# Optimization experiments

Hardware: AMD Instinct MI355X
Metric: run time of the kernel (lower is better)

## Reference

```python
import jax, jax.numpy as jnp
import numpy as np

B, N, M = 16, 4096, 256
Q_DIM, CTX_DIM = 512, 768
HEADS, DIM_HEAD = 8, 64
INNER = HEADS * DIM_HEAD
SCALE = DIM_HEAD ** -0.5


def setup_inputs() -> dict:
    key = jax.random.key(0)
    ks = jax.random.split(key, 8)
    x = jax.random.normal(ks[0], (B, N, Q_DIM), dtype=jnp.float32)
    obj_txt = jax.random.normal(ks[1], (B, M, CTX_DIM), dtype=jnp.float32)
    obj_mask = jax.random.randint(ks[2], (B, N, M), 0, 2) > 0
    obj_vector = jnp.ones((B, M), dtype=bool)  # all-True keeps output finite (see notes)
    Wq = jax.random.normal(ks[3], (Q_DIM, INNER), dtype=jnp.float32) * 0.02
    Wk = jax.random.normal(ks[4], (CTX_DIM, INNER), dtype=jnp.float32) * 0.02
    Wv = jax.random.normal(ks[5], (CTX_DIM, INNER), dtype=jnp.float32) * 0.02
    Wo = jax.random.normal(ks[6], (INNER, Q_DIM), dtype=jnp.float32) * 0.02
    bo = jnp.zeros((Q_DIM,), dtype=jnp.float32)
    return {"x": x, "obj_txt": obj_txt, "obj_mask": obj_mask, "obj_vector": obj_vector,
            "Wq": Wq, "Wk": Wk, "Wv": Wv, "Wo": Wo, "bo": bo}


def reference(x, obj_txt, obj_mask, obj_vector, Wq, Wk, Wv, Wo, bo):
    b, n, _ = x.shape
    m = obj_txt.shape[1]
    q = (x @ Wq).reshape(b, n, HEADS, DIM_HEAD)          # [B,N,H,C]
    k = (obj_txt @ Wk).reshape(b, m, HEADS, DIM_HEAD)    # [B,M,H,C]
    v = (obj_txt @ Wv).reshape(b, m, HEADS, DIM_HEAD)
    sim = jnp.einsum('bnhc,bmhc->bhnm', q, k) * SCALE    # [B,H,N,M]
    neg = -jnp.finfo(sim.dtype).max
    # pre-softmax mask (obj_vector broadcasts over heads and queries)
    sim = jnp.where(obj_vector[:, None, None, :], sim, neg)
    # NOTE: original computes sim.softmax(-1) but then discards it, using the
    # pre-softmax masked sim with ~obj_mask positions set to 0 as the attention.
    attn = jnp.where(obj_mask[:, None, :, :], sim, jnp.array(0.0, sim.dtype))
    out = jnp.einsum('bhnm,bmhc->bnhc', attn, v).reshape(b, n, INNER)
    return out @ Wo + bo
```

## Files before the change

### kernel.cpp

```cpp
#include <hip/hip_runtime.h>

typedef unsigned short u16;
typedef unsigned char u8;
typedef unsigned int u32;
typedef unsigned long long u64;
typedef __attribute__((ext_vector_type(4))) float floatx4;
typedef __attribute__((ext_vector_type(8))) __bf16 bf16x8;

#define GLD_LDS(SRC, DST) __builtin_amdgcn_global_load_lds( \
    (const __attribute__((address_space(1))) void*)(SRC),   \
    (__attribute__((address_space(3))) void*)(DST), 16, 0, 0)

static __device__ __forceinline__ u16 f2bf(float f) {
  return __builtin_bit_cast(u16, (__bf16)f);
}
static __device__ __forceinline__ u32 pk2bf(float a, float b) {
  return (u32)f2bf(a) | ((u32)f2bf(b) << 16);
}
static __device__ __forceinline__ floatx4 mfma16(bf16x8 a, bf16x8 b, floatx4 c) {
  return __builtin_amdgcn_mfma_f32_16x16x32_bf16(a, b, c, 0, 0, 0);
}


__global__ void detect_mask_kernel(const unsigned int* __restrict__ m, int* __restrict__ flag) {
  __shared__ int sh[4];
  int t = threadIdx.x;
  int any = 0;
  for (int i = t; i < 16384; i += 256) any |= ((m[i] & 0xFFFFFF00u) != 0u) ? 1 : 0;
  unsigned long long b = __ballot(any != 0);
  if ((t & 63) == 0) sh[t >> 6] = (b != 0ull) ? 1 : 0;
  __syncthreads();
  if (t == 0) flag[0] = (sh[0] | sh[1] | sh[2] | sh[3]);
}

__global__ void prep_weights_kernel(const float* __restrict__ Wq, const float* __restrict__ Wk,
                                    const float* __restrict__ Wv, const float* __restrict__ Wo,
                                    u16* __restrict__ WqT, u16* __restrict__ WkT,
                                    u16* __restrict__ WvT, u16* __restrict__ WoT) {
  int z = blockIdx.y;
  const float* src = (z == 0) ? Wq : (z == 1) ? Wk : (z == 2) ? Wv : Wo;
  u16* dst = (z == 0) ? WqT : (z == 1) ? WkT : (z == 2) ? WvT : WoT;
  int K = (z == 1 || z == 2) ? 768 : 512;
  int total = K * 512;
  int idx = blockIdx.x * 256 + threadIdx.x;
  if (idx >= total) return;
  int n = idx / K, k = idx - n * K;
  float v = src[(size_t)k * 512 + n];
  if (z == 0) v *= 0.125f;
  dst[idx] = f2bf(v);
}

__global__ __launch_bounds__(256) void gemm_qkv_kernel(
    const float* __restrict__ A, const u16* __restrict__ Bt0, const u16* __restrict__ Bt1,
    u16* __restrict__ C0, u16* __restrict__ C1, int Nn, int K, int kvmode) {
  const u16* Bt = Bt0;
  u16* Cout = C0;
  int mode = 0;
  if (kvmode && blockIdx.z == 1) { Bt = Bt1; Cout = C1; mode = 2; }
  __shared__ float Asf[2][4096];
  __shared__ u16 Bs[2][4096];
  int m0 = blockIdx.x * 128, n0 = blockIdx.y * 128;
  int t = threadIdx.x, lane = t & 63;
  int w = t >> 6, wr = w >> 1, wc = w & 1, lr = lane & 15, lg = lane >> 4;
  floatx4 acc[4][4];
#pragma unroll
  for (int i = 0; i < 4; ++i)
#pragma unroll
    for (int j = 0; j < 4; ++j) acc[i][j] = (floatx4){0.f, 0.f, 0.f, 0.f};
  int nk = K >> 5;

  auto stage = [&](int kt, int bf) {
    int k0 = kt * 32;
#pragma unroll
    for (int i = 0; i < 4; ++i) {
      int idx = (i * 4 + w) * 64 + lane;
      int row = idx >> 3, g = idx & 7;
      int gs = g ^ (row & 7);
      const float* src = A + (size_t)(m0 + row) * K + k0 + gs * 4;
      char* dst = ((char*)&Asf[0][0]) + bf * 16384 + (i * 4 + w) * 1024;
      GLD_LDS(src, dst);
    }
#pragma unroll
    for (int i = 0; i < 2; ++i) {
      int idx = (i * 4 + w) * 64 + lane;
      int row = idx >> 2, g = idx & 3;
      int gs = g ^ ((row >> 1) & 3);
      const u16* src = Bt + (size_t)(n0 + row) * K + k0 + gs * 8;
      char* dst = ((char*)&Bs[0][0]) + bf * 8192 + (i * 4 + w) * 1024;
      GLD_LDS(src, dst);
    }
  };

  stage(0, 0);
  __syncthreads();
  for (int kt = 0; kt < nk; ++kt) {
    int cur = kt & 1;
    if (kt + 1 < nk) stage(kt + 1, cur ^ 1);
    bf16x8 av[4];
#pragma unroll
    for (int i = 0; i < 4; ++i) {
      int r = wr * 64 + i * 16 + lr;
      int g0 = (2 * lg) ^ (r & 7), g1 = (2 * lg + 1) ^ (r & 7);
      float4 f0 = *reinterpret_cast<const float4*>(&Asf[cur][r * 32 + g0 * 4]);
      float4 f1 = *reinterpret_cast<const float4*>(&Asf[cur][r * 32 + g1 * 4]);
      bf16x8 pk;
      pk[0] = (__bf16)f0.x; pk[1] = (__bf16)f0.y; pk[2] = (__bf16)f0.z; pk[3] = (__bf16)f0.w;
      pk[4] = (__bf16)f1.x; pk[5] = (__bf16)f1.y; pk[6] = (__bf16)f1.z; pk[7] = (__bf16)f1.w;
      av[i] = pk;
    }
#pragma unroll
    for (int j = 0; j < 4; ++j) {
      int rb = wc * 64 + j * 16 + lr;
      int gb = lg ^ ((rb >> 1) & 3);
      bf16x8 bv = *reinterpret_cast<const bf16x8*>(&Bs[cur][rb * 32 + gb * 8]);
#pragma unroll
      for (int i = 0; i < 4; ++i) acc[i][j] = mfma16(bv, av[i], acc[i][j]);
    }
    __syncthreads();
  }
#pragma unroll
  for (int i = 0; i < 4; ++i)
#pragma unroll
    for (int j = 0; j < 4; ++j) {
      int n_row = m0 + wr * 64 + i * 16 + lr;
      int colb = n0 + wc * 64 + j * 16 + lg * 4;
      if (mode == 0) {
        ushort4 pk4;
        pk4.x = f2bf(acc[i][j][0]); pk4.y = f2bf(acc[i][j][1]);
        pk4.z = f2bf(acc[i][j][2]); pk4.w = f2bf(acc[i][j][3]);
        *reinterpret_cast<ushort4*>(&Cout[(size_t)n_row * Nn + colb]) = pk4;
      } else {
        int bb = n_row >> 8, mm = n_row & 255;
#pragma unroll
        for (int r = 0; r < 4; ++r) {
          int col = colb + r;
          int hh = col >> 6, cc = col & 63;
          Cout[(((size_t)(bb * 8 + hh)) * 64 + cc) * 256 + mm] = f2bf(acc[i][j][r]);
        }
      }
    }
}

__global__ __launch_bounds__(256) void gemm_o_kernel(
    const u16* __restrict__ A, const u16* __restrict__ Bt, const float* __restrict__ bo,
    float* __restrict__ out) {
  __shared__ u16 As[2][4096];
  __shared__ u16 Bs[2][4096];
  int m0 = blockIdx.x * 128, n0 = blockIdx.y * 128;
  int t = threadIdx.x, lane = t & 63;
  int w = t >> 6, wr = w >> 1, wc = w & 1, lr = lane & 15, lg = lane >> 4;
  floatx4 acc[4][4];
#pragma unroll
  for (int i = 0; i < 4; ++i)
#pragma unroll
    for (int j = 0; j < 4; ++j) acc[i][j] = (floatx4){0.f, 0.f, 0.f, 0.f};

  auto stage = [&](int kt, int bf) {
    int k0 = kt * 32;
#pragma unroll
    for (int i = 0; i < 2; ++i) {
      int idx = (i * 4 + w) * 64 + lane;
      int row = idx >> 2, g = idx & 3;
      int gs = g ^ ((row >> 1) & 3);
      const u16* srcA = A + (size_t)(m0 + row) * 512 + k0 + gs * 8;
      char* dstA = ((char*)&As[0][0]) + bf * 8192 + (i * 4 + w) * 1024;
      GLD_LDS(srcA, dstA);
      const u16* srcB = Bt + (size_t)(n0 + row) * 512 + k0 + gs * 8;
      char* dstB = ((char*)&Bs[0][0]) + bf * 8192 + (i * 4 + w) * 1024;
      GLD_LDS(srcB, dstB);
    }
  };

  stage(0, 0);
  __syncthreads();
  for (int kt = 0; kt < 16; ++kt) {
    int cur = kt & 1;
    if (kt + 1 < 16) stage(kt + 1, cur ^ 1);
    bf16x8 av[4];
#pragma unroll
    for (int i = 0; i < 4; ++i) {
      int r = wr * 64 + i * 16 + lr;
      int ga = lg ^ ((r >> 1) & 3);
      av[i] = *reinterpret_cast<const bf16x8*>(&As[cur][r * 32 + ga * 8]);
    }
#pragma unroll
    for (int j = 0; j < 4; ++j) {
      int rb = wc * 64 + j * 16 + lr;
      int gb = lg ^ ((rb >> 1) & 3);
      bf16x8 bv = *reinterpret_cast<const bf16x8*>(&Bs[cur][rb * 32 + gb * 8]);
#pragma unroll
      for (int i = 0; i < 4; ++i) acc[i][j] = mfma16(bv, av[i], acc[i][j]);
    }
    __syncthreads();
  }
#pragma unroll
  for (int i = 0; i < 4; ++i)
#pragma unroll
    for (int j = 0; j < 4; ++j) {
      int n_row = m0 + wr * 64 + i * 16 + lr;
      int colb = n0 + wc * 64 + j * 16 + lg * 4;
      float4 bv4 = *reinterpret_cast<const float4*>(&bo[colb]);
      float4 st;
      st.x = acc[i][j][0] + bv4.x; st.y = acc[i][j][1] + bv4.y;
      st.z = acc[i][j][2] + bv4.z; st.w = acc[i][j][3] + bv4.w;
      *reinterpret_cast<float4*>(&out[(size_t)n_row * 512 + colb]) = st;
    }
}

__global__ __launch_bounds__(256, 2) void attn_kernel(
    u16* qoin, const u16* __restrict__ Kb, const u16* __restrict__ Vt,
    const void* __restrict__ maskp, const int* __restrict__ flag) {
  __shared__ u16 k_lds[16384];
  __shared__ u16 v_lds[16384];
  __shared__ u16 ubuf[4][1024];
  int id = blockIdx.y * 32 + blockIdx.x;
  int xcd = id & 7, j0 = id >> 3;
  int bIdx = 2 * xcd + (j0 >> 5);
  int nx = j0 & 31;
  int t = threadIdx.x, lane = t & 63, w = t >> 6, lr = lane & 15, lg = lane >> 4;
  int n0w = nx * 128 + w * 32;
  bool mByte = flag[0] != 0;

  u64 mb[2];
#pragma unroll
  for (int nt = 0; nt < 2; ++nt) {
    int n = n0w + nt * 16 + lr;
    size_t base = ((size_t)(bIdx * 4096 + n)) * 256;
    u64 bits = 0;
    if (mByte) {
      const u8* mp = (const u8*)maskp + base;
      for (int mt = 0; mt < 16; ++mt) {
        u32 dw = *(const u32*)(mp + mt * 16 + lg * 4);
#pragma unroll
        for (int r = 0; r < 4; ++r)
          if ((dw >> (8 * r)) & 0xFFu) bits |= (1ull << (mt * 4 + r));
      }
    } else {
      const int* mp = (const int*)maskp + base;
      for (int mt = 0; mt < 16; ++mt) {
        int4 q = *(const int4*)(mp + mt * 16 + lg * 4);
        if (q.x) bits |= 1ull << (mt * 4 + 0);
        if (q.y) bits |= 1ull << (mt * 4 + 1);
        if (q.z) bits |= 1ull << (mt * 4 + 2);
        if (q.w) bits |= 1ull << (mt * 4 + 3);
      }
    }
    mb[nt] = bits;
  }

  for (int h = 0; h < 8; ++h) {
    __syncthreads();
#pragma unroll
    for (int i = 0; i < 8; ++i) {
      int m = i * 32 + (t >> 3);
      int gs = (t & 7) ^ (m & 7);
      const u16* src = Kb + ((size_t)(bIdx * 256 + m)) * 512 + h * 64 + gs * 8;
      char* dst = ((char*)k_lds) + i * 4096 + w * 1024;
      GLD_LDS(src, dst);
    }
#pragma unroll
    for (int i = 0; i < 8; ++i) {
      int c = i * 8 + (t >> 5);
      int g = t & 31;
      int gs = (g & 24) | ((g & 7) ^ (c & 7));
      const u16* src = Vt + (((size_t)(bIdx * 8 + h)) * 64 + c) * 256 + gs * 8;
      char* dst = ((char*)v_lds) + i * 4096 + w * 1024;
      GLD_LDS(src, dst);
    }
    bf16x8 qf[2][2];
#pragma unroll
    for (int nt = 0; nt < 2; ++nt)
#pragma unroll
      for (int ks = 0; ks < 2; ++ks)
        qf[nt][ks] = *reinterpret_cast<const bf16x8*>(
            qoin + ((size_t)(bIdx * 4096 + n0w + nt * 16 + lr)) * 512 + h * 64 + ks * 32 + lg * 8);
    __syncthreads();

    floatx4 acc2[2][4];
#pragma unroll
    for (int nt = 0; nt < 2; ++nt)
#pragma unroll
      for (int ct = 0; ct < 4; ++ct) acc2[nt][ct] = (floatx4){0.f, 0.f, 0.f, 0.f};

    for (int ch = 0; ch < 8; ++ch) {
      floatx4 s[2][2];
#pragma unroll
      for (int nt = 0; nt < 2; ++nt)
#pragma unroll
        for (int mt2 = 0; mt2 < 2; ++mt2) s[nt][mt2] = (floatx4){0.f, 0.f, 0.f, 0.f};
#pragma unroll
      for (int mt2 = 0; mt2 < 2; ++mt2) {
        int m = (ch * 2 + mt2) * 16 + lr;
        bf16x8 af[2];
#pragma unroll
        for (int ks = 0; ks < 2; ++ks) {
          int g = ks * 4 + lg;
          af[ks] = *reinterpret_cast<const bf16x8*>(&k_lds[m * 64 + ((g ^ (m & 7)) << 3)]);
        }
#pragma unroll
        for (int nt = 0; nt < 2; ++nt) {
          s[nt][mt2] = mfma16(af[0], qf[nt][0], s[nt][mt2]);
          s[nt][mt2] = mfma16(af[1], qf[nt][1], s[nt][mt2]);
        }
      }
      u32* pb = (u32*)&ubuf[w][0];
#pragma unroll
      for (int nt = 0; nt < 2; ++nt)
#pragma unroll
        for (int mt2 = 0; mt2 < 2; ++mt2) {
          int sh = (ch * 2 + mt2) * 4;
          float v0 = ((mb[nt] >> (sh + 0)) & 1ull) ? s[nt][mt2][0] : 0.f;
          float v1 = ((mb[nt] >> (sh + 1)) & 1ull) ? s[nt][mt2][1] : 0.f;
          float v2 = ((mb[nt] >> (sh + 2)) & 1ull) ? s[nt][mt2][2] : 0.f;
          float v3 = ((mb[nt] >> (sh + 3)) & 1ull) ? s[nt][mt2][3] : 0.f;
          int gm = mt2 * 4 + lg;
          int gmp = gm ^ ((lr & 3) << 1);
          u64 pkd = (u64)pk2bf(v0, v1) | ((u64)pk2bf(v2, v3) << 32);
          *(u64*)(pb + nt * 256 + lr * 16 + gmp * 2) = pkd;
        }
      bf16x8 pf[2];
#pragma unroll
      for (int nt = 0; nt < 2; ++nt) {
        int gmp = (2 * lg) ^ ((lr & 3) << 1);
        pf[nt] = *reinterpret_cast<const bf16x8*>(&ubuf[w][nt * 512 + lr * 32 + gmp * 4]);
      }
#pragma unroll
      for (int ct = 0; ct < 4; ++ct) {
        int c = ct * 16 + lr;
        int gv = ch * 4 + lg;
        int gvp = (gv & 24) | ((gv & 7) ^ (c & 7));
        bf16x8 vf = *reinterpret_cast<const bf16x8*>(&v_lds[c * 256 + gvp * 8]);
#pragma unroll
        for (int nt = 0; nt < 2; ++nt) acc2[nt][ct] = mfma16(pf[nt], vf, acc2[nt][ct]);
      }
    }

#pragma unroll
    for (int nt = 0; nt < 2; ++nt) {
#pragma unroll
      for (int ct = 0; ct < 4; ++ct)
#pragma unroll
        for (int r = 0; r < 4; ++r) {
          int c = ct * 16 + lr;
          int n = lg * 4 + r;
          int cg = c >> 3;
          ubuf[w][n * 64 + ((cg ^ (n & 7)) << 3) + (c & 7)] = f2bf(acc2[nt][ct][r]);
        }
#pragma unroll
      for (int half = 0; half < 2; ++half) {
        int np = (lane >> 3) + half * 8;
        int cc = lane & 7;
        bf16x8 frag = *reinterpret_cast<const bf16x8*>(&ubuf[w][np * 64 + ((cc ^ (np & 7)) << 3)]);
        *reinterpret_cast<bf16x8*>(
            qoin + ((size_t)(bIdx * 4096 + n0w + nt * 16 + np)) * 512 + h * 64 + cc * 8) = frag;
      }
    }
  }
}

extern "C" void kernel_launch(void* const* d_in, const int* in_sizes, int n_in,
                              void* d_out, int out_size, void* d_ws, size_t ws_size,
                              hipStream_t stream) {
  const float* x = (const float*)d_in[0];
  const float* obj_txt = (const float*)d_in[1];
  const void* obj_mask = d_in[2];
  const float* Wq = (const float*)d_in[4];
  const float* Wk = (const float*)d_in[5];
  const float* Wv = (const float*)d_in[6];
  const float* Wo = (const float*)d_in[7];
  const float* bo = (const float*)d_in[8];
  float* out = (float*)d_out;

  char* ws = (char*)d_ws;
  u16* Qb = (u16*)ws;
  u16* Kb = (u16*)(ws + 67108864);
  u16* Vt = (u16*)(ws + 71303168);
  u16* WqT = (u16*)(ws + 75497472);
  u16* WkT = (u16*)(ws + 76021760);
  u16* WvT = (u16*)(ws + 76808192);
  u16* WoT = (u16*)(ws + 77594624);
  int* flag = (int*)(ws + 78118912);

  detect_mask_kernel<<<1, 256, 0, stream>>>((const unsigned int*)obj_mask, flag);
  prep_weights_kernel<<<dim3(1536, 4, 1), 256, 0, stream>>>(Wq, Wk, Wv, Wo, WqT, WkT, WvT, WoT);
  gemm_qkv_kernel<<<dim3(512, 4, 1), 256, 0, stream>>>(x, WqT, nullptr, Qb, nullptr, 512, 512, 0);
  gemm_qkv_kernel<<<dim3(32, 4, 2), 256, 0, stream>>>(obj_txt, WkT, WvT, Kb, Vt, 512, 768, 1);
  attn_kernel<<<dim3(32, 16, 1), 256, 0, stream>>>(Qb, Kb, Vt, obj_mask, flag);
  gemm_o_kernel<<<dim3(512, 4, 1), 256, 0, stream>>>(Qb, WoT, bo, out);
}
```

Baseline: 307.9 us.

## Widen Q/O GEMM tiles to 128x256 and use 8 waves in attention

The Q-projection and output GEMMs now use 128x256 output tiles per block (8 accumulator columns per wave), which halves the number of times each A row tile is reloaded and converted. This costs more accumulator registers and LDS per block. The attention kernel moves from 4 waves each handling 32 queries to 8 waves each handling 16 queries, so each K/V tile staged per head is shared by more waves. The KV GEMM is split into its own kernel with constant K.

```diff
diff --git a/kernel.cpp b/kernel.cpp
--- a/kernel.cpp
+++ b/kernel.cpp
@@ -50,24 +50,19 @@
   dst[idx] = f2bf(v);
 }
 
-__global__ __launch_bounds__(256) void gemm_qkv_kernel(
-    const float* __restrict__ A, const u16* __restrict__ Bt0, const u16* __restrict__ Bt1,
-    u16* __restrict__ C0, u16* __restrict__ C1, int Nn, int K, int kvmode) {
-  const u16* Bt = Bt0;
-  u16* Cout = C0;
-  int mode = 0;
-  if (kvmode && blockIdx.z == 1) { Bt = Bt1; Cout = C1; mode = 2; }
+__global__ __launch_bounds__(256) void gemm_q_kernel(
+    const float* __restrict__ A, const u16* __restrict__ Bt, u16* __restrict__ Cout) {
   __shared__ float Asf[2][4096];
-  __shared__ u16 Bs[2][4096];
-  int m0 = blockIdx.x * 128, n0 = blockIdx.y * 128;
+  __shared__ u16 Bs[2][8192];
+  int bid = blockIdx.x;
+  int m0 = (bid >> 1) * 128, n0 = (bid & 1) * 256;
   int t = threadIdx.x, lane = t & 63;
   int w = t >> 6, wr = w >> 1, wc = w & 1, lr = lane & 15, lg = lane >> 4;
-  floatx4 acc[4][4];
-#pragma unroll
-  for (int i = 0; i < 4; ++i)
-#pragma unroll
-    for (int j = 0; j < 4; ++j) acc[i][j] = (floatx4){0.f, 0.f, 0.f, 0.f};
-  int nk = K >> 5;
+  floatx4 acc[4][8];
+#pragma unroll
+  for (int i = 0; i < 4; ++i)
+#pragma unroll
+    for (int j = 0; j < 8; ++j) acc[i][j] = (floatx4){0.f, 0.f, 0.f, 0.f};
 
   auto stage = [&](int kt, int bf) {
     int k0 = kt * 32;
@@ -76,26 +71,26 @@
       int idx = (i * 4 + w) * 64 + lane;
       int row = idx >> 3, g = idx & 7;
       int gs = g ^ (row & 7);
-      const float* src = A + (size_t)(m0 + row) * K + k0 + gs * 4;
+      const float* src = A + (size_t)(m0 + row) * 512 + k0 + gs * 4;
       char* dst = ((char*)&Asf[0][0]) + bf * 16384 + (i * 4 + w) * 1024;
       GLD_LDS(src, dst);
     }
 #pragma unroll
-    for (int i = 0; i < 2; ++i) {
+    for (int i = 0; i < 4; ++i) {
       int idx = (i * 4 + w) * 64 + lane;
       int row = idx >> 2, g = idx & 3;
       int gs = g ^ ((row >> 1) & 3);
-      const u16* src = Bt + (size_t)(n0 + row) * K + k0 + gs * 8;
-      char* dst = ((char*)&Bs[0][0]) + bf * 8192 + (i * 4 + w) * 1024;
+      const u16* src = Bt + (size_t)(n0 + row) * 512 + k0 + gs * 8;
+      char* dst = ((char*)&Bs[0][0]) + bf * 16384 + (i * 4 + w) * 1024;
       GLD_LDS(src, dst);
     }
   };
 
   stage(0, 0);
   __syncthreads();
-  for (int kt = 0; kt < nk; ++kt) {
+  for (int kt = 0; kt < 16; ++kt) {
     int cur = kt & 1;
-    if (kt + 1 < nk) stage(kt + 1, cur ^ 1);
+    if (kt + 1 < 16) stage(kt + 1, cur ^ 1);
     bf16x8 av[4];
 #pragma unroll
     for (int i = 0; i < 4; ++i) {
@@ -109,6 +104,86 @@
       av[i] = pk;
     }
 #pragma unroll
+    for (int j = 0; j < 8; ++j) {
+      int rb = wc * 128 + j * 16 + lr;
+      int gb = lg ^ ((rb >> 1) & 3);
+      bf16x8 bv = *reinterpret_cast<const bf16x8*>(&Bs[cur][rb * 32 + gb * 8]);
+#pragma unroll
+      for (int i = 0; i < 4; ++i) acc[i][j] = mfma16(bv, av[i], acc[i][j]);
+    }
+    __syncthreads();
+  }
+#pragma unroll
+  for (int i = 0; i < 4; ++i)
+#pragma unroll
+    for (int j = 0; j < 8; ++j) {
+      int n_row = m0 + wr * 64 + i * 16 + lr;
+      int colb = n0 + wc * 128 + j * 16 + lg * 4;
+      ushort4 pk4;
+      pk4.x = f2bf(acc[i][j][0]); pk4.y = f2bf(acc[i][j][1]);
+      pk4.z = f2bf(acc[i][j][2]); pk4.w = f2bf(acc[i][j][3]);
+      *reinterpret_cast<ushort4*>(&Cout[(size_t)n_row * 512 + colb]) = pk4;
+    }
+}
+
+__global__ __launch_bounds__(256) void gemm_kv_kernel(
+    const float* __restrict__ A, const u16* __restrict__ Bt0, const u16* __restrict__ Bt1,
+    u16* __restrict__ C0, u16* __restrict__ C1) {
+  const u16* Bt = Bt0;
+  u16* Cout = C0;
+  int mode = 0;
+  if (blockIdx.z == 1) { Bt = Bt1; Cout = C1; mode = 2; }
+  __shared__ float Asf[2][4096];
+  __shared__ u16 Bs[2][4096];
+  int m0 = blockIdx.x * 128, n0 = blockIdx.y * 128;
+  int t = threadIdx.x, lane = t & 63;
+  int w = t >> 6, wr = w >> 1, wc = w & 1, lr = lane & 15, lg = lane >> 4;
+  floatx4 acc[4][4];
+#pragma unroll
+  for (int i = 0; i < 4; ++i)
+#pragma unroll
+    for (int j = 0; j < 4; ++j) acc[i][j] = (floatx4){0.f, 0.f, 0.f, 0.f};
+
+  auto stage = [&](int kt, int bf) {
+    int k0 = kt * 32;
+#pragma unroll
+    for (int i = 0; i < 4; ++i) {
+      int idx = (i * 4 + w) * 64 + lane;
+      int row = idx >> 3, g = idx & 7;
+      int gs = g ^ (row & 7);
+      const float* src = A + (size_t)(m0 + row) * 768 + k0 + gs * 4;
+      char* dst = ((char*)&Asf[0][0]) + bf * 16384 + (i * 4 + w) * 1024;
+      GLD_LDS(src, dst);
+    }
+#pragma unroll
+    for (int i = 0; i < 2; ++i) {
+      int idx = (i * 4 + w) * 64 + lane;
+      int row = idx >> 2, g = idx & 3;
+      int gs = g ^ ((row >> 1) & 3);
+      const u16* src = Bt + (size_t)(n0 + row) * 768 + k0 + gs * 8;
+      char* dst = ((char*)&Bs[0][0]) + bf * 8192 + (i * 4 + w) * 1024;
+      GLD_LDS(src, dst);
+    }
+  };
+
+  stage(0, 0);
+  __syncthreads();
+  for (int kt = 0; kt < 24; ++kt) {
+    int cur = kt & 1;
+    if (kt + 1 < 24) stage(kt + 1, cur ^ 1);
+    bf16x8 av[4];
+#pragma unroll
+    for (int i = 0; i < 4; ++i) {
+      int r = wr * 64 + i * 16 + lr;
+      int g0 = (2 * lg) ^ (r & 7), g1 = (2 * lg + 1) ^ (r & 7);
+      float4 f0 = *reinterpret_cast<const float4*>(&Asf[cur][r * 32 + g0 * 4]);
+      float4 f1 = *reinterpret_cast<const float4*>(&Asf[cur][r * 32 + g1 * 4]);
+      bf16x8 pk;
+      pk[0] = (__bf16)f0.x; pk[1] = (__bf16)f0.y; pk[2] = (__bf16)f0.z; pk[3] = (__bf16)f0.w;
+      pk[4] = (__bf16)f1.x; pk[5] = (__bf16)f1.y; pk[6] = (__bf16)f1.z; pk[7] = (__bf16)f1.w;
+      av[i] = pk;
+    }
+#pragma unroll
     for (int j = 0; j < 4; ++j) {
       int rb = wc * 64 + j * 16 + lr;
       int gb = lg ^ ((rb >> 1) & 3);
@@ -128,7 +203,7 @@
         ushort4 pk4;
         pk4.x = f2bf(acc[i][j][0]); pk4.y = f2bf(acc[i][j][1]);
         pk4.z = f2bf(acc[i][j][2]); pk4.w = f2bf(acc[i][j][3]);
-        *reinterpret_cast<ushort4*>(&Cout[(size_t)n_row * Nn + colb]) = pk4;
+        *reinterpret_cast<ushort4*>(&Cout[(size_t)n_row * 512 + colb]) = pk4;
       } else {
         int bb = n_row >> 8, mm = n_row & 255;
 #pragma unroll
@@ -145,15 +220,16 @@
     const u16* __restrict__ A, const u16* __restrict__ Bt, const float* __restrict__ bo,
     float* __restrict__ out) {
   __shared__ u16 As[2][4096];
-  __shared__ u16 Bs[2][4096];
-  int m0 = blockIdx.x * 128, n0 = blockIdx.y * 128;
+  __shared__ u16 Bs[2][8192];
+  int bid = blockIdx.x;
+  int m0 = (bid >> 1) * 128, n0 = (bid & 1) * 256;
   int t = threadIdx.x, lane = t & 63;
   int w = t >> 6, wr = w >> 1, wc = w & 1, lr = lane & 15, lg = lane >> 4;
-  floatx4 acc[4][4];
-#pragma unroll
-  for (int i = 0; i < 4; ++i)
-#pragma unroll
-    for (int j = 0; j < 4; ++j) acc[i][j] = (floatx4){0.f, 0.f, 0.f, 0.f};
+  floatx4 acc[4][8];
+#pragma unroll
+  for (int i = 0; i < 4; ++i)
+#pragma unroll
+    for (int j = 0; j < 8; ++j) acc[i][j] = (floatx4){0.f, 0.f, 0.f, 0.f};
 
   auto stage = [&](int kt, int bf) {
     int k0 = kt * 32;
@@ -162,12 +238,18 @@
       int idx = (i * 4 + w) * 64 + lane;
       int row = idx >> 2, g = idx & 3;
       int gs = g ^ ((row >> 1) & 3);
-      const u16* srcA = A + (size_t)(m0 + row) * 512 + k0 + gs * 8;
-      char* dstA = ((char*)&As[0][0]) + bf * 8192 + (i * 4 + w) * 1024;
-      GLD_LDS(srcA, dstA);
-      const u16* srcB = Bt + (size_t)(n0 + row) * 512 + k0 + gs * 8;
-      char* dstB = ((char*)&Bs[0][0]) + bf * 8192 + (i * 4 + w) * 1024;
-      GLD_LDS(srcB, dstB);
+      const u16* src = A + (size_t)(m0 + row) * 512 + k0 + gs * 8;
+      char* dst = ((char*)&As[0][0]) + bf * 8192 + (i * 4 + w) * 1024;
+      GLD_LDS(src, dst);
+    }
+#pragma unroll
+    for (int i = 0; i < 4; ++i) {
+      int idx = (i * 4 + w) * 64 + lane;
+      int row = idx >> 2, g = idx & 3;
+      int gs = g ^ ((row >> 1) & 3);
+      const u16* src = Bt + (size_t)(n0 + row) * 512 + k0 + gs * 8;
+      char* dst = ((char*)&Bs[0][0]) + bf * 16384 + (i * 4 + w) * 1024;
+      GLD_LDS(src, dst);
     }
   };
 
@@ -184,8 +266,8 @@
       av[i] = *reinterpret_cast<const bf16x8*>(&As[cur][r * 32 + ga * 8]);
     }
 #pragma unroll
-    for (int j = 0; j < 4; ++j) {
-      int rb = wc * 64 + j * 16 + lr;
+    for (int j = 0; j < 8; ++j) {
+      int rb = wc * 128 + j * 16 + lr;
       int gb = lg ^ ((rb >> 1) & 3);
       bf16x8 bv = *reinterpret_cast<const bf16x8*>(&Bs[cur][rb * 32 + gb * 8]);
 #pragma unroll
@@ -196,9 +278,9 @@
 #pragma unroll
   for (int i = 0; i < 4; ++i)
 #pragma unroll
-    for (int j = 0; j < 4; ++j) {
+    for (int j = 0; j < 8; ++j) {
       int n_row = m0 + wr * 64 + i * 16 + lr;
-      int colb = n0 + wc * 64 + j * 16 + lg * 4;
+      int colb = n0 + wc * 128 + j * 16 + lg * 4;
       float4 bv4 = *reinterpret_cast<const float4*>(&bo[colb]);
       float4 st;
       st.x = acc[i][j][0] + bv4.x; st.y = acc[i][j][1] + bv4.y;
@@ -207,24 +289,23 @@
     }
 }
 
-__global__ __launch_bounds__(256, 2) void attn_kernel(
+__global__ __launch_bounds__(512, 2) void attn_kernel(
     u16* qoin, const u16* __restrict__ Kb, const u16* __restrict__ Vt,
     const void* __restrict__ maskp, const int* __restrict__ flag) {
   __shared__ u16 k_lds[16384];
   __shared__ u16 v_lds[16384];
-  __shared__ u16 ubuf[4][1024];
+  __shared__ u16 ubuf[8][1024];
   int id = blockIdx.y * 32 + blockIdx.x;
   int xcd = id & 7, j0 = id >> 3;
   int bIdx = 2 * xcd + (j0 >> 5);
   int nx = j0 & 31;
-  int t = threadIdx.x, lane = t & 63, w = t >> 6, lr = lane & 15, lg = lane >> 4;
-  int n0w = nx * 128 + w * 32;
+  int lane = threadIdx.x & 63, w = threadIdx.x >> 6, lr = lane & 15, lg = lane >> 4;
+  int n0w = nx * 128 + w * 16;
   bool mByte = flag[0] != 0;
 
-  u64 mb[2];
-#pragma unroll
-  for (int nt = 0; nt < 2; ++nt) {
-    int n = n0w + nt * 16 + lr;
+  u64 mb;
+  {
+    int n = n0w + lr;
     size_t base = ((size_t)(bIdx * 4096 + n)) * 256;
     u64 bits = 0;
     if (mByte) {
@@ -245,115 +326,95 @@
         if (q.w) bits |= 1ull << (mt * 4 + 3);
       }
     }
-    mb[nt] = bits;
+    mb = bits;
   }
 
   for (int h = 0; h < 8; ++h) {
     __syncthreads();
 #pragma unroll
-    for (int i = 0; i < 8; ++i) {
-      int m = i * 32 + (t >> 3);
-      int gs = (t & 7) ^ (m & 7);
+    for (int i = 0; i < 4; ++i) {
+      int idx = (i * 8 + w) * 64 + lane;
+      int m = idx >> 3, g = idx & 7;
+      int gs = g ^ (m & 7);
       const u16* src = Kb + ((size_t)(bIdx * 256 + m)) * 512 + h * 64 + gs * 8;
-      char* dst = ((char*)k_lds) + i * 4096 + w * 1024;
-      GLD_LDS(src, dst);
-    }
-#pragma unroll
-    for (int i = 0; i < 8; ++i) {
-      int c = i * 8 + (t >> 5);
-      int g = t & 31;
+      char* dst = ((char*)k_lds) + (i * 8 + w) * 1024;
+      GLD_LDS(src, dst);
+    }
+#pragma unroll
+    for (int i = 0; i < 4; ++i) {
+      int idx = (i * 8 + w) * 64 + lane;
+      int c = idx >> 5, g = idx & 31;
       int gs = (g & 24) | ((g & 7) ^ (c & 7));
       const u16* src = Vt + (((size_t)(bIdx * 8 + h)) * 64 + c) * 256 + gs * 8;
-      char* dst = ((char*)v_lds) + i * 4096 + w * 1024;
-      GLD_LDS(src, dst);
-    }
-    bf16x8 qf[2][2];
-#pragma unroll
-    for (int nt = 0; nt < 2; ++nt)
-#pragma unroll
-      for (int ks = 0; ks < 2; ++ks)
-        qf[nt][ks] = *reinterpret_cast<const bf16x8*>(
-            qoin + ((size_t)(bIdx * 4096 + n0w + nt * 16 + lr)) * 512 + h * 64 + ks * 32 + lg * 8);
+      char* dst = ((char*)v_lds) + (i * 8 + w) * 1024;
+      GLD_LDS(src, dst);
+    }
+    bf16x8 qf[2];
+#pragma unroll
+    for (int ks = 0; ks < 2; ++ks)
+      qf[ks] = *reinterpret_cast<const bf16x8*>(
+          qoin + ((size_t)(bIdx * 4096 + n0w + lr)) * 512 + h * 64 + ks * 32 + lg * 8);
     __syncthreads();
 
-    floatx4 acc2[2][4];
-#pragma unroll
-    for (int nt = 0; nt < 2; ++nt)
-#pragma unroll
-      for (int ct = 0; ct < 4; ++ct) acc2[nt][ct] = (floatx4){0.f, 0.f, 0.f, 0.f};
+    floatx4 acc2[4];
+#pragma unroll
+    for (int ct = 0; ct < 4; ++ct) acc2[ct] = (floatx4){0.f, 0.f, 0.f, 0.f};
 
     for (int ch = 0; ch < 8; ++ch) {
-      floatx4 s[2][2];
-#pragma unroll
-      for (int nt = 0; nt < 2; ++nt)
-#pragma unroll
-        for (int mt2 = 0; mt2 < 2; ++mt2) s[nt][mt2] = (floatx4){0.f, 0.f, 0.f, 0.f};
+      floatx4 s[2];
+#pragma unroll
+      for (int mt2 = 0; mt2 < 2; ++mt2) s[mt2] = (floatx4){0.f, 0.f, 0.f, 0.f};
 #pragma unroll
       for (int mt2 = 0; mt2 < 2; ++mt2) {
         int m = (ch * 2 + mt2) * 16 + lr;
-        bf16x8 af[2];
 #pragma unroll
         for (int ks = 0; ks < 2; ++ks) {
           int g = ks * 4 + lg;
-          af[ks] = *reinterpret_cast<const bf16x8*>(&k_lds[m * 64 + ((g ^ (m & 7)) << 3)]);
+          bf16x8 af = *reinterpret_cast<const bf16x8*>(&k_lds[m * 64 + ((g ^ (m & 7)) << 3)]);
+          s[mt2] = mfma16(af, qf[ks], s[mt2]);
         }
-#pragma unroll
-        for (int nt = 0; nt < 2; ++nt) {
-          s[nt][mt2] = mfma16(af[0], qf[nt][0], s[nt][mt2]);
-          s[nt][mt2] = mfma16(af[1], qf[nt][1], s[nt][mt2]);
-        }
       }
       u32* pb = (u32*)&ubuf[w][0];
 #pragma unroll
-      for (int nt = 0; nt < 2; ++nt)
-#pragma unroll
-        for (int mt2 = 0; mt2 < 2; ++mt2) {
-          int sh = (ch * 2 + mt2) * 4;
-          float v0 = ((mb[nt] >> (sh + 0)) & 1ull) ? s[nt][mt2][0] : 0.f;
-          float v1 = ((mb[nt] >> (sh + 1)) & 1ull) ? s[nt][mt2][1] : 0.f;
-          float v2 = ((mb[nt] >> (sh + 2)) & 1ull) ? s[nt][mt2][2] : 0.f;
-          float v3 = ((mb[nt] >> (sh + 3)) & 1ull) ? s[nt][mt2][3] : 0.f;
-          int gm = mt2 * 4 + lg;
-          int gmp = gm ^ ((lr & 3) << 1);
-          u64 pkd = (u64)pk2bf(v0, v1) | ((u64)pk2bf(v2, v3) << 32);
-          *(u64*)(pb + nt * 256 + lr * 16 + gmp * 2) = pkd;
-        }
-      bf16x8 pf[2];
-#pragma unroll
-      for (int nt = 0; nt < 2; ++nt) {
-        int gmp = (2 * lg) ^ ((lr & 3) << 1);
-        pf[nt] = *reinterpret_cast<const bf16x8*>(&ubuf[w][nt * 512 + lr * 32 + gmp * 4]);
-      }
+      for (int mt2 = 0; mt2 < 2; ++mt2) {
+        int sh = (ch * 2 + mt2) * 4;
+        float v0 = ((mb >> (sh + 0)) & 1ull) ? s[mt2][0] : 0.f;
+        float v1 = ((mb >> (sh + 1)) & 1ull) ? s[mt2][1] : 0.f;
+        float v2 = ((mb >> (sh + 2)) & 1ull) ? s[mt2][2] : 0.f;
+        float v3 = ((mb >> (sh + 3)) & 1ull) ? s[mt2][3] : 0.f;
+        int gm = mt2 * 4 + lg;
+        int gmp = gm ^ ((lr & 3) << 1);
+        u64 pkd = (u64)pk2bf(v0, v1) | ((u64)pk2bf(v2, v3) << 32);
+        *(u64*)(pb + lr * 16 + gmp * 2) = pkd;
+      }
+      int gmp = (2 * lg) ^ ((lr & 3) << 1);
+      bf16x8 pf = *reinterpret_cast<const bf16x8*>(&ubuf[w][lr * 32 + gmp * 4]);
 #pragma unroll
       for (int ct = 0; ct < 4; ++ct) {
         int c = ct * 16 + lr;
         int gv = ch * 4 + lg;
         int gvp = (gv & 24) | ((gv & 7) ^ (c & 7));
         bf16x8 vf = *reinterpret_cast<const bf16x8*>(&v_lds[c * 256 + gvp * 8]);
-#pragma unroll
-        for (int nt = 0; nt < 2; ++nt) acc2[nt][ct] = mfma16(pf[nt], vf, acc2[nt][ct]);
-      }
-    }
-
-#pragma unroll
-    for (int nt = 0; nt < 2; ++nt) {
-#pragma unroll
-      for (int ct = 0; ct < 4; ++ct)
-#pragma unroll
-        for (int r = 0; r < 4; ++r) {
-          int c = ct * 16 + lr;
-          int n = lg * 4 + r;
-          int cg = c >> 3;
-          ubuf[w][n * 64 + ((cg ^ (n & 7)) << 3) + (c & 7)] = f2bf(acc2[nt][ct][r]);
-        }
-#pragma unroll
-      for (int half = 0; half < 2; ++half) {
-        int np = (lane >> 3) + half * 8;
-        int cc = lane & 7;
-        bf16x8 frag = *reinterpret_cast<const bf16x8*>(&ubuf[w][np * 64 + ((cc ^ (np & 7)) << 3)]);
-        *reinterpret_cast<bf16x8*>(
-            qoin + ((size_t)(bIdx * 4096 + n0w + nt * 16 + np)) * 512 + h * 64 + cc * 8) = frag;
-      }
+        acc2[ct] = mfma16(pf, vf, acc2[ct]);
+      }
+    }
+
+#pragma unroll
+    for (int ct = 0; ct < 4; ++ct)
+#pragma unroll
+      for (int r = 0; r < 4; ++r) {
+        int c = ct * 16 + lr;
+        int n = lg * 4 + r;
+        int cg = c >> 3;
+        ubuf[w][n * 64 + ((cg ^ (n & 7)) << 3) + (c & 7)] = f2bf(acc2[ct][r]);
+      }
+#pragma unroll
+    for (int half = 0; half < 2; ++half) {
+      int np = (lane >> 3) + half * 8;
+      int cc = lane & 7;
+      bf16x8 frag = *reinterpret_cast<const bf16x8*>(&ubuf[w][np * 64 + ((cc ^ (np & 7)) << 3)]);
+      *reinterpret_cast<bf16x8*>(
+          qoin + ((size_t)(bIdx * 4096 + n0w + np)) * 512 + h * 64 + cc * 8) = frag;
     }
   }
 }
@@ -383,8 +444,8 @@
 
   detect_mask_kernel<<<1, 256, 0, stream>>>((const unsigned int*)obj_mask, flag);
   prep_weights_kernel<<<dim3(1536, 4, 1), 256, 0, stream>>>(Wq, Wk, Wv, Wo, WqT, WkT, WvT, WoT);
-  gemm_qkv_kernel<<<dim3(512, 4, 1), 256, 0, stream>>>(x, WqT, nullptr, Qb, nullptr, 512, 512, 0);
-  gemm_qkv_kernel<<<dim3(32, 4, 2), 256, 0, stream>>>(obj_txt, WkT, WvT, Kb, Vt, 512, 768, 1);
-  attn_kernel<<<dim3(32, 16, 1), 256, 0, stream>>>(Qb, Kb, Vt, obj_mask, flag);
-  gemm_o_kernel<<<dim3(512, 4, 1), 256, 0, stream>>>(Qb, WoT, bo, out);
-}
+  gemm_q_kernel<<<1024, 256, 0, stream>>>(x, WqT, Qb);
+  gemm_kv_kernel<<<dim3(32, 4, 2), 256, 0, stream>>>(obj_txt, WkT, WvT, Kb, Vt);
+  attn_kernel<<<dim3(32, 16, 1), 512, 0, stream>>>(Qb, Kb, Vt, obj_mask, flag);
+  gemm_o_kernel<<<1024, 256, 0, stream>>>(Qb, WoT, bo, out);
+}
```

Result: no change. 304.4 us (-1.2%).
